# Performance work log

Hardware: AMD Instinct MI355X
Metric: run time of the kernel (lower is better)

Reference implementation:

```python
import jax, jax.numpy as jnp
import numpy as np

B, N, D = 4, 512, 128
NEG = -1e9


def setup_inputs() -> dict:
    key = jax.random.key(0)
    ks = jax.random.split(key, 11)
    s = 1.0 / np.sqrt(D)
    inp = {
        "q": jax.random.normal(ks[0], (B, N, D), jnp.float32),
        "k": jax.random.normal(ks[1], (B, N, D), jnp.float32),
        "v": jax.random.normal(ks[2], (B, N, D), jnp.float32),
        "mask": jnp.ones((B, N), jnp.int32),
        # nn.Linear params: weight [out,in], bias [out]
        "Wq": jax.random.uniform(ks[3], (D, D), jnp.float32, -s, s),
        "bq": jax.random.uniform(ks[4], (D,), jnp.float32, -s, s),
        "Wk": jax.random.uniform(ks[5], (D, D), jnp.float32, -s, s),
        "bk": jax.random.uniform(ks[6], (D,), jnp.float32, -s, s),
        "Wv": jax.random.uniform(ks[7], (D, D), jnp.float32, -s, s),
        "bv": jax.random.uniform(ks[8], (D,), jnp.float32, -s, s),
        "Wo": jax.random.uniform(ks[9], (D, D), jnp.float32, -s, s),
        "bo": jax.random.uniform(ks[10], (D,), jnp.float32, -s, s),
    }
    return inp


def reference(q, k, v, mask, Wq, bq, Wk, bk, Wv, bv, Wo, bo):
    # linear projections (torch Linear: x @ W.T + b)
    qp = jnp.einsum('bnd,ed->bne', q, Wq) + bq
    kp = jnp.einsum('bnd,ed->bne', k, Wk) + bk
    vp = jnp.einsum('bnd,ed->bne', v, Wv) + bv
    # outer-product attention: scores [b, n, m, d]
    scores = jnp.einsum('bnd,bmd->bnmd', qp, kp)
    # mask [b, n] -> [b, n, 1, 1], fill masked positions with -1e9
    scores = jnp.where(mask[:, :, None, None] == 0, NEG, scores)
    # per-channel softmax over m (axis=2); dropout is a no-op at inference
    scores = jax.nn.softmax(scores, axis=2)
    out = jnp.einsum('bnmd,bmd->bnd', scores, vp)
    return jnp.einsum('bnd,ed->bne', out, Wo) + bo
```

## Files before the change

### kernel.cpp

```cpp
#include <hip/hip_runtime.h>

#define BB 4
#define NN 512
#define DD 128
#define RR 8

static constexpr float LOG2E = 1.4426950408889634f;
#define EXP2F(x) __builtin_amdgcn_exp2f(x)

__global__ __launch_bounds__(256) void wtrans_kernel(
    const float* __restrict__ Wq, const float* __restrict__ Wk,
    const float* __restrict__ Wv, const float* __restrict__ Wo,
    float* __restrict__ WT)
{
    const int l = blockIdx.x * 256 + threadIdx.x;
    const int m = l >> 14;
    const int e = (l >> 7) & (DD - 1);
    const int j = l & (DD - 1);
    const float* W = (m == 0) ? Wq : (m == 1) ? Wk : (m == 2) ? Wv : Wo;
    WT[(m << 14) + j * DD + e] = W[e * DD + j];
}

__global__ __launch_bounds__(128) void proj_kernel(
    const float* __restrict__ q, const float* __restrict__ k,
    const float* __restrict__ v, const float* __restrict__ WT,
    const float* __restrict__ bq, const float* __restrict__ bk,
    const float* __restrict__ bv,
    float* __restrict__ qpT, float* __restrict__ kpT, float* __restrict__ vpT)
{
    const int e  = threadIdx.x;
    const int t  = blockIdx.y;
    const int g0 = blockIdx.x * RR;

    const float* x    = (t == 0) ? q   : (t == 1) ? k   : v;
    const float* wt   = WT + (t << 14);
    const float* bias = (t == 0) ? bq  : (t == 1) ? bk  : bv;
    float*       outp = (t == 0) ? qpT : (t == 1) ? kpT : vpT;
    const float scale = (t == 0) ? LOG2E : 1.0f;

    float acc[RR];
    #pragma unroll
    for (int r = 0; r < RR; ++r) acc[r] = 0.f;

    #pragma unroll 4
    for (int j4 = 0; j4 < DD / 4; ++j4) {
        const float w0 = wt[(j4 * 4 + 0) * DD + e];
        const float w1 = wt[(j4 * 4 + 1) * DD + e];
        const float w2 = wt[(j4 * 4 + 2) * DD + e];
        const float w3 = wt[(j4 * 4 + 3) * DD + e];
        #pragma unroll
        for (int r = 0; r < RR; ++r) {
            const float4 xr = *(const float4*)(x + (g0 + r) * DD + j4 * 4);
            acc[r] = fmaf(xr.x, w0, fmaf(xr.y, w1, fmaf(xr.z, w2, fmaf(xr.w, w3, acc[r]))));
        }
    }

    const float be = bias[e];
    #pragma unroll
    for (int r = 0; r < RR; ++r) {
        const int g = g0 + r;
        const int b = g >> 9;
        const int n = g & (NN - 1);
        outp[(b * DD + e) * NN + n] = (acc[r] + be) * scale;
    }
}

__global__ __launch_bounds__(512) void attn_kernel(
    const float* __restrict__ qpT, const float* __restrict__ kpT,
    const float* __restrict__ vpT, const int* __restrict__ mask,
    float* __restrict__ att)
{
    const int bd = blockIdx.x;
    const int b  = bd >> 7;
    const int d  = bd & (DD - 1);
    const int n  = threadIdx.x;

    float qv = qpT[bd * NN + n];
    if (mask[b * NN + n] == 0) qv = 0.f;

    const float4* kc = (const float4*)(kpT + bd * NN);
    const float4* vc = (const float4*)(vpT + bd * NN);

    float n0 = 0.f, n1 = 0.f, n2 = 0.f, n3 = 0.f;
    float d0 = 0.f, d1 = 0.f;
    #pragma unroll 8
    for (int m4 = 0; m4 < NN / 4; ++m4) {
        const float4 k4 = kc[m4];
        const float4 v4 = vc[m4];
        const float p0 = EXP2F(qv * k4.x);
        const float p1 = EXP2F(qv * k4.y);
        const float p2 = EXP2F(qv * k4.z);
        const float p3 = EXP2F(qv * k4.w);
        n0 = fmaf(p0, v4.x, n0);
        n1 = fmaf(p1, v4.y, n1);
        n2 = fmaf(p2, v4.z, n2);
        n3 = fmaf(p3, v4.w, n3);
        d0 += p0 + p1;
        d1 += p2 + p3;
    }

    att[(b * NN + n) * DD + d] = ((n0 + n1) + (n2 + n3)) / (d0 + d1);
}

__global__ __launch_bounds__(128) void outproj_kernel(
    const float* __restrict__ att, const float* __restrict__ WT,
    const float* __restrict__ bo, float* __restrict__ out)
{
    const int e  = threadIdx.x;
    const int g0 = blockIdx.x * RR;
    const float* wt = WT + (3 << 14);

    float acc[RR];
    #pragma unroll
    for (int r = 0; r < RR; ++r) acc[r] = 0.f;

    #pragma unroll 4
    for (int j4 = 0; j4 < DD / 4; ++j4) {
        const float w0 = wt[(j4 * 4 + 0) * DD + e];
        const float w1 = wt[(j4 * 4 + 1) * DD + e];
        const float w2 = wt[(j4 * 4 + 2) * DD + e];
        const float w3 = wt[(j4 * 4 + 3) * DD + e];
        #pragma unroll
        for (int r = 0; r < RR; ++r) {
            const float4 a = *(const float4*)(att + (g0 + r) * DD + j4 * 4);
            acc[r] = fmaf(a.x, w0, fmaf(a.y, w1, fmaf(a.z, w2, fmaf(a.w, w3, acc[r]))));
        }
    }

    const float boe = bo[e];
    #pragma unroll
    for (int r = 0; r < RR; ++r)
        out[(g0 + r) * DD + e] = acc[r] + boe;
}

extern "C" void kernel_launch(void* const* d_in, const int* in_sizes, int n_in,
                              void* d_out, int out_size, void* d_ws, size_t ws_size,
                              hipStream_t stream)
{
    const float* q    = (const float*)d_in[0];
    const float* k    = (const float*)d_in[1];
    const float* v    = (const float*)d_in[2];
    const int*   mask = (const int*)  d_in[3];
    const float* Wq   = (const float*)d_in[4];
    const float* bq   = (const float*)d_in[5];
    const float* Wk   = (const float*)d_in[6];
    const float* bk   = (const float*)d_in[7];
    const float* Wv   = (const float*)d_in[8];
    const float* bv   = (const float*)d_in[9];
    const float* Wo   = (const float*)d_in[10];
    const float* bo   = (const float*)d_in[11];
    float* out = (float*)d_out;

    float* ws  = (float*)d_ws;
    float* qpT = ws;
    float* kpT = ws + 1 * BB * DD * NN;
    float* vpT = ws + 2 * BB * DD * NN;
    float* att = ws + 3 * BB * DD * NN;
    float* WT  = ws + 4 * BB * DD * NN;

    wtrans_kernel<<<4 * DD * DD / 256, 256, 0, stream>>>(Wq, Wk, Wv, Wo, WT);

    dim3 pgrid(BB * NN / RR, 3);
    proj_kernel<<<pgrid, 128, 0, stream>>>(q, k, v, WT, bq, bk, bv, qpT, kpT, vpT);

    attn_kernel<<<BB * DD, 512, 0, stream>>>(qpT, kpT, vpT, mask, att);

    outproj_kernel<<<BB * NN / RR, 128, 0, stream>>>(att, WT, bo, out);
}
```

Measured before the change: 133.6 us.

## Pack transposed weights as float4, split rows across subgroups, stage K/V in LDS

The weight transpose now writes a float4-interleaved layout, so each projection thread loads four weights with one vector load. The projection and output-projection kernels move to 512-thread blocks, each 128-thread subgroup handling two rows or one row, to raise parallelism and cut per-thread register pressure. The attention kernel stages the K and V columns in shared memory before the exp loop, instead of having every thread read them from global memory. This reduces weight reuse per thread and adds a block barrier in attention.

```diff
diff --git a/kernel.cpp b/kernel.cpp
--- a/kernel.cpp
+++ b/kernel.cpp
@@ -3,7 +3,6 @@
 #define BB 4
 #define NN 512
 #define DD 128
-#define RR 8
 
 static constexpr float LOG2E = 1.4426950408889634f;
 #define EXP2F(x) __builtin_amdgcn_exp2f(x)
@@ -11,57 +10,56 @@
 __global__ __launch_bounds__(256) void wtrans_kernel(
     const float* __restrict__ Wq, const float* __restrict__ Wk,
     const float* __restrict__ Wv, const float* __restrict__ Wo,
-    float* __restrict__ WT)
+    float* __restrict__ WTp)
 {
     const int l = blockIdx.x * 256 + threadIdx.x;
-    const int m = l >> 14;
+    const int t = l >> 14;
     const int e = (l >> 7) & (DD - 1);
     const int j = l & (DD - 1);
-    const float* W = (m == 0) ? Wq : (m == 1) ? Wk : (m == 2) ? Wv : Wo;
-    WT[(m << 14) + j * DD + e] = W[e * DD + j];
+    const float* W = (t == 0) ? Wq : (t == 1) ? Wk : (t == 2) ? Wv : Wo;
+    WTp[(t << 14) + (j >> 2) * (DD * 4) + e * 4 + (j & 3)] = W[e * DD + j];
 }
 
-__global__ __launch_bounds__(128) void proj_kernel(
+__global__ __launch_bounds__(512) void proj_kernel(
     const float* __restrict__ q, const float* __restrict__ k,
-    const float* __restrict__ v, const float* __restrict__ WT,
+    const float* __restrict__ v, const float* __restrict__ WTp,
     const float* __restrict__ bq, const float* __restrict__ bk,
     const float* __restrict__ bv,
     float* __restrict__ qpT, float* __restrict__ kpT, float* __restrict__ vpT)
 {
-    const int e  = threadIdx.x;
-    const int t  = blockIdx.y;
-    const int g0 = blockIdx.x * RR;
+    const int t   = blockIdx.y;
+    const int e   = threadIdx.x & (DD - 1);
+    const int sub = threadIdx.x >> 7;
+    const int g0  = blockIdx.x * 8 + sub * 2;
 
-    const float* x    = (t == 0) ? q   : (t == 1) ? k   : v;
-    const float* wt   = WT + (t << 14);
-    const float* bias = (t == 0) ? bq  : (t == 1) ? bk  : bv;
-    float*       outp = (t == 0) ? qpT : (t == 1) ? kpT : vpT;
-    const float scale = (t == 0) ? LOG2E : 1.0f;
+    const float*  x    = (t == 0) ? q   : (t == 1) ? k   : v;
+    const float4* wt4  = (const float4*)(WTp + (t << 14));
+    const float*  bias = (t == 0) ? bq  : (t == 1) ? bk  : bv;
+    float*        outp = (t == 0) ? qpT : (t == 1) ? kpT : vpT;
+    const float scale  = (t == 0) ? LOG2E : 1.0f;
 
-    float acc[RR];
-    #pragma unroll
-    for (int r = 0; r < RR; ++r) acc[r] = 0.f;
+    const float4* x0 = (const float4*)(x + g0 * DD);
+    const float4* x1 = (const float4*)(x + (g0 + 1) * DD);
 
-    #pragma unroll 4
+    float a0 = 0.f, a1 = 0.f;
+    #pragma unroll 8
     for (int j4 = 0; j4 < DD / 4; ++j4) {
-        const float w0 = wt[(j4 * 4 + 0) * DD + e];
-        const float w1 = wt[(j4 * 4 + 1) * DD + e];
-        const float w2 = wt[(j4 * 4 + 2) * DD + e];
-        const float w3 = wt[(j4 * 4 + 3) * DD + e];
-        #pragma unroll
-        for (int r = 0; r < RR; ++r) {
-            const float4 xr = *(const float4*)(x + (g0 + r) * DD + j4 * 4);
-            acc[r] = fmaf(xr.x, w0, fmaf(xr.y, w1, fmaf(xr.z, w2, fmaf(xr.w, w3, acc[r]))));
-        }
+        const float4 w  = wt4[j4 * DD + e];
+        const float4 r0 = x0[j4];
+        const float4 r1 = x1[j4];
+        a0 = fmaf(r0.x, w.x, fmaf(r0.y, w.y, fmaf(r0.z, w.z, fmaf(r0.w, w.w, a0))));
+        a1 = fmaf(r1.x, w.x, fmaf(r1.y, w.y, fmaf(r1.z, w.z, fmaf(r1.w, w.w, a1))));
     }
 
     const float be = bias[e];
-    #pragma unroll
-    for (int r = 0; r < RR; ++r) {
-        const int g = g0 + r;
-        const int b = g >> 9;
-        const int n = g & (NN - 1);
-        outp[(b * DD + e) * NN + n] = (acc[r] + be) * scale;
+    {
+        const int b = g0 >> 9, n = g0 & (NN - 1);
+        outp[(b * DD + e) * NN + n] = (a0 + be) * scale;
+    }
+    {
+        const int g = g0 + 1;
+        const int b = g >> 9, n = g & (NN - 1);
+        outp[(b * DD + e) * NN + n] = (a1 + be) * scale;
     }
 }
 
@@ -70,23 +68,30 @@
     const float* __restrict__ vpT, const int* __restrict__ mask,
     float* __restrict__ att)
 {
+    __shared__ float sk[NN];
+    __shared__ float sv[NN];
+
     const int bd = blockIdx.x;
     const int b  = bd >> 7;
     const int d  = bd & (DD - 1);
     const int n  = threadIdx.x;
 
+    sk[n] = kpT[bd * NN + n];
+    sv[n] = vpT[bd * NN + n];
+
     float qv = qpT[bd * NN + n];
     if (mask[b * NN + n] == 0) qv = 0.f;
+    __syncthreads();
 
-    const float4* kc = (const float4*)(kpT + bd * NN);
-    const float4* vc = (const float4*)(vpT + bd * NN);
+    const float4* k4p = (const float4*)sk;
+    const float4* v4p = (const float4*)sv;
 
     float n0 = 0.f, n1 = 0.f, n2 = 0.f, n3 = 0.f;
     float d0 = 0.f, d1 = 0.f;
     #pragma unroll 8
     for (int m4 = 0; m4 < NN / 4; ++m4) {
-        const float4 k4 = kc[m4];
-        const float4 v4 = vc[m4];
+        const float4 k4 = k4p[m4];
+        const float4 v4 = v4p[m4];
         const float p0 = EXP2F(qv * k4.x);
         const float p1 = EXP2F(qv * k4.y);
         const float p2 = EXP2F(qv * k4.z);
@@ -102,35 +107,26 @@
     att[(b * NN + n) * DD + d] = ((n0 + n1) + (n2 + n3)) / (d0 + d1);
 }
 
-__global__ __launch_bounds__(128) void outproj_kernel(
-    const float* __restrict__ att, const float* __restrict__ WT,
+__global__ __launch_bounds__(512) void outproj_kernel(
+    const float* __restrict__ att, const float* __restrict__ WTp,
     const float* __restrict__ bo, float* __restrict__ out)
 {
-    const int e  = threadIdx.x;
-    const int g0 = blockIdx.x * RR;
-    const float* wt = WT + (3 << 14);
+    const int e   = threadIdx.x & (DD - 1);
+    const int sub = threadIdx.x >> 7;
+    const int g   = blockIdx.x * 4 + sub;
 
-    float acc[RR];
-    #pragma unroll
-    for (int r = 0; r < RR; ++r) acc[r] = 0.f;
+    const float4* wt4 = (const float4*)(WTp + (3 << 14));
+    const float4* xr  = (const float4*)(att + g * DD);
 
-    #pragma unroll 4
+    float acc = 0.f;
+    #pragma unroll 8
     for (int j4 = 0; j4 < DD / 4; ++j4) {
-        const float w0 = wt[(j4 * 4 + 0) * DD + e];
-        const float w1 = wt[(j4 * 4 + 1) * DD + e];
-        const float w2 = wt[(j4 * 4 + 2) * DD + e];
-        const float w3 = wt[(j4 * 4 + 3) * DD + e];
-        #pragma unroll
-        for (int r = 0; r < RR; ++r) {
-            const float4 a = *(const float4*)(att + (g0 + r) * DD + j4 * 4);
-            acc[r] = fmaf(a.x, w0, fmaf(a.y, w1, fmaf(a.z, w2, fmaf(a.w, w3, acc[r]))));
-        }
+        const float4 w = wt4[j4 * DD + e];
+        const float4 a = xr[j4];
+        acc = fmaf(a.x, w.x, fmaf(a.y, w.y, fmaf(a.z, w.z, fmaf(a.w, w.w, acc))));
     }
 
-    const float boe = bo[e];
-    #pragma unroll
-    for (int r = 0; r < RR; ++r)
-        out[(g0 + r) * DD + e] = acc[r] + boe;
+    out[g * DD + e] = acc + bo[e];
 }
 
 extern "C" void kernel_launch(void* const* d_in, const int* in_sizes, int n_in,
@@ -156,14 +152,14 @@
     float* kpT = ws + 1 * BB * DD * NN;
     float* vpT = ws + 2 * BB * DD * NN;
     float* att = ws + 3 * BB * DD * NN;
-    float* WT  = ws + 4 * BB * DD * NN;
+    float* WTp = ws + 4 * BB * DD * NN;
 
-    wtrans_kernel<<<4 * DD * DD / 256, 256, 0, stream>>>(Wq, Wk, Wv, Wo, WT);
+    wtrans_kernel<<<4 * DD * DD / 256, 256, 0, stream>>>(Wq, Wk, Wv, Wo, WTp);
 
-    dim3 pgrid(BB * NN / RR, 3);
-    proj_kernel<<<pgrid, 128, 0, stream>>>(q, k, v, WT, bq, bk, bv, qpT, kpT, vpT);
+    dim3 pgrid(BB * NN / 8, 3);
+    proj_kernel<<<pgrid, 512, 0, stream>>>(q, k, v, WTp, bq, bk, bv, qpT, kpT, vpT);
 
     attn_kernel<<<BB * DD, 512, 0, stream>>>(qpT, kpT, vpT, mask, att);
 
-    outproj_kernel<<<BB * NN / RR, 128, 0, stream>>>(att, WT, bo, out);
+    outproj_kernel<<<BB * NN / 4, 512, 0, stream>>>(att, WTp, bo, out);
 }
```

Result: faster. 130.7 us (-2.1%).
